# Optimization experiments

Measured on AMD Instinct MI355X. Metric: run time of the kernel, lower is better.

## Reference

```python
import jax, jax.numpy as jnp
import numpy as np

EMBED_DIM = 1024
NUM_HEADS = 16
HEAD_DIM = EMBED_DIM // NUM_HEADS
SCALING = (1.0 / HEAD_DIM) ** 0.5


def setup_inputs() -> dict:
    key = jax.random.key(0)
    ks = jax.random.split(key, 9)
    d = EMBED_DIM
    return {
        "hidden_states": jax.random.normal(ks[0], (4, 2048, d), dtype=jnp.float32),
        "q_w": jax.random.normal(ks[1], (d, d), dtype=jnp.float32) * 0.02,
        "q_b": jax.random.normal(ks[2], (d,), dtype=jnp.float32) * 0.02,
        "k_w": jax.random.normal(ks[3], (d, d), dtype=jnp.float32) * 0.02,
        "k_b": jax.random.normal(ks[4], (d,), dtype=jnp.float32) * 0.02,
        "v_w": jax.random.normal(ks[5], (d, d), dtype=jnp.float32) * 0.02,
        "v_b": jax.random.normal(ks[6], (d,), dtype=jnp.float32) * 0.02,
        "out_w": jax.random.normal(ks[7], (d, d), dtype=jnp.float32) * 0.02,
        "out_b": jax.random.normal(ks[8], (d,), dtype=jnp.float32) * 0.02,
    }


def _shape(x, bsz, seq, nh, hd):
    # [B, T, E] -> [B, H, T, Hd]
    return x.reshape(bsz, seq, nh, hd).transpose(0, 2, 1, 3)


def reference(hidden_states, q_w, q_b, k_w, k_b, v_w, v_b, out_w, out_b):
    bsz, tgt_len, _ = hidden_states.shape
    # torch Linear: y = x @ W.T + b; query scaled by sqrt(1/head_dim)
    q = (hidden_states @ q_w.T + q_b) * SCALING
    k = hidden_states @ k_w.T + k_b
    v = hidden_states @ v_w.T + v_b
    q = _shape(q, bsz, tgt_len, NUM_HEADS, HEAD_DIM)
    k = _shape(k, bsz, tgt_len, NUM_HEADS, HEAD_DIM)
    v = _shape(v, bsz, tgt_len, NUM_HEADS, HEAD_DIM)
    # [B, H, T, S]
    attn_weights = jnp.einsum("bhtd,bhsd->bhts", q, k)
    attn_weights = jax.nn.softmax(attn_weights, axis=-1)
    # [B, H, T, Hd] -> [B, T, E]
    attn_output = jnp.einsum("bhts,bhsd->bhtd", attn_weights, v)
    attn_output = attn_output.transpose(0, 2, 1, 3).reshape(bsz, tgt_len, EMBED_DIM)
    return attn_output @ out_w.T + out_b
```

## Files before the change

### kernel.cpp

```cpp
#include <hip/hip_runtime.h>
#include <hip/hip_bf16.h>
#include <cstdint>
#include <math.h>

typedef uint16_t u16;
typedef __attribute__((ext_vector_type(8))) short short8;
typedef __attribute__((ext_vector_type(2))) float floatx2;
typedef __attribute__((ext_vector_type(4))) float floatx4;
typedef __attribute__((ext_vector_type(16))) float floatx16;

__device__ __forceinline__ float bf2f(u16 u) {
  return __uint_as_float(((uint32_t)u) << 16);
}
__device__ __forceinline__ u16 f2bf(float f) {
  uint32_t u = __float_as_uint(f);
  u += 0x7FFF + ((u >> 16) & 1);
  return (u16)(u >> 16);
}

#if __has_builtin(__builtin_amdgcn_exp2f)
#define EXP2(x) __builtin_amdgcn_exp2f(x)
#else
#define EXP2(x) exp2f(x)
#endif

__device__ __forceinline__ void glds16(const void* g, void* l) {
  __builtin_amdgcn_global_load_lds(
      (const __attribute__((address_space(1))) void*)g,
      (__attribute__((address_space(3))) void*)l, 16, 0, 0);
}

__device__ __forceinline__ bool detect_fp32(const u16* __restrict__ hs) {
  int big = 0;
#pragma unroll
  for (int i = 0; i < 128; ++i) {
    const int e = (hs[i] >> 7) & 0xFF;
    big += (e >= 140);
  }
  return big > 0;
}

__device__ __forceinline__ void conv_blk(
    const void* __restrict__ src, u16* __restrict__ dst, int i, bool f32)
{
  if (f32) {
    const float4 v = ((const float4*)src)[i];
    ushort4 d;
    d.x = f2bf(v.x); d.y = f2bf(v.y); d.z = f2bf(v.z); d.w = f2bf(v.w);
    ((ushort4*)dst)[i] = d;
  } else {
    ((ushort4*)dst)[i] = ((const ushort4*)src)[i];
  }
}

__global__ __launch_bounds__(256) void convert_all(
    const void* __restrict__ hs, const void* __restrict__ qw,
    const void* __restrict__ kw, const void* __restrict__ vw,
    const void* __restrict__ ow, const void* __restrict__ qb,
    const void* __restrict__ kb, const void* __restrict__ vb,
    const void* __restrict__ ob,
    u16* __restrict__ d_hs, u16* __restrict__ d_qw, u16* __restrict__ d_kw,
    u16* __restrict__ d_vw, u16* __restrict__ d_ow, u16* __restrict__ d_qb,
    u16* __restrict__ d_kb, u16* __restrict__ d_vb, u16* __restrict__ d_ob)
{
  const bool f32 = detect_fp32((const u16*)hs);
  const int bid = blockIdx.x;
  const int tid = threadIdx.x;
  if (bid < 2048) {
#pragma unroll
    for (int k = 0; k < 4; ++k)
      conv_blk(hs, d_hs, bid * 1024 + k * 256 + tid, f32);
  } else if (bid < 2048 + 1024) {
    const int w = (bid - 2048) >> 8;
    const int base = ((bid - 2048) & 255) * 1024;
    const void* s = (w == 0) ? qw : (w == 1) ? kw : (w == 2) ? vw : ow;
    u16* d        = (w == 0) ? d_qw : (w == 1) ? d_kw : (w == 2) ? d_vw : d_ow;
#pragma unroll
    for (int k = 0; k < 4; ++k)
      conv_blk(s, d, base + k * 256 + tid, f32);
  } else {
    const int w = bid - 3072;
    const void* s = (w == 0) ? qb : (w == 1) ? kb : (w == 2) ? vb : ob;
    u16* d        = (w == 0) ? d_qb : (w == 1) ? d_kb : (w == 2) ? d_vb : d_ob;
    conv_blk(s, d, tid, f32);
  }
}

template <int MODE>
__device__ __forceinline__ void gemm_body(
    const u16* __restrict__ A, const u16* __restrict__ W,
    const u16* __restrict__ bias, void* __restrict__ vout,
    float scale, u16* As, u16* Bs, int bx, int by, bool f32out)
{
  constexpr int KD = 1024;
  const int tid  = threadIdx.x;
  const int lane = tid & 63;
  const int l15  = lane & 15;
  const int quad = lane >> 4;
  const int wid  = tid >> 6;
  const int bm = by * 256, bn = bx * 128;
  const int wm = (wid >> 1) * 64, wn = (wid & 1) * 64;

  floatx4 acc[4][4];
#pragma unroll
  for (int i = 0; i < 4; ++i)
#pragma unroll
    for (int j = 0; j < 4; ++j)
#pragma unroll
      for (int r = 0; r < 4; ++r) acc[i][j][r] = 0.0f;

  const u16* Ag0 = A + (size_t)(bm + (tid >> 2)) * KD + (tid & 3) * 8;
  const u16* Ag1 = Ag0 + (size_t)128 * KD;
  const u16* Wg0 = W + (size_t)(bn + (tid >> 2)) * KD + (tid & 3) * 8;
  u16* AsD = As + tid * 8;
  u16* BsD = Bs + tid * 8;

  for (int kt = 0; kt < KD / 64; ++kt) {
    const int ko = kt * 64;
    glds16(Ag0 + ko,      AsD);
    glds16(Ag1 + ko,      AsD + 4096);
    glds16(Wg0 + ko,      BsD);
    glds16(Ag0 + ko + 32, AsD + 8192);
    glds16(Ag1 + ko + 32, AsD + 8192 + 4096);
    glds16(Wg0 + ko + 32, BsD + 4096);
    __syncthreads();
#pragma unroll
    for (int h = 0; h < 2; ++h) {
      const u16* Ah = As + h * 8192;
      const u16* Bh = Bs + h * 4096;
      short8 af[4], bf[4];
#pragma unroll
      for (int mb = 0; mb < 4; ++mb)
        af[mb] = *(const short8*)&Ah[(wm + mb * 16 + l15) * 32 + quad * 8];
#pragma unroll
      for (int nb = 0; nb < 4; ++nb)
        bf[nb] = *(const short8*)&Bh[(wn + nb * 16 + l15) * 32 + quad * 8];
#pragma unroll
      for (int mb = 0; mb < 4; ++mb)
#pragma unroll
        for (int nb = 0; nb < 4; ++nb) {
          if (MODE == 2)
            acc[mb][nb] = __builtin_amdgcn_mfma_f32_16x16x32_bf16(
                bf[nb], af[mb], acc[mb][nb], 0, 0, 0);
          else
            acc[mb][nb] = __builtin_amdgcn_mfma_f32_16x16x32_bf16(
                af[mb], bf[nb], acc[mb][nb], 0, 0, 0);
        }
    }
    __syncthreads();
  }

  if (MODE == 2) {
#pragma unroll
    for (int nb = 0; nb < 4; ++nb)
#pragma unroll
      for (int r = 0; r < 4; ++r) {
        const int wrow = bn + wn + nb * 16 + quad * 4 + r;
        const float bv = bf2f(bias[wrow]);
        const int h = wrow >> 6, d = wrow & 63;
        u16* out = (u16*)vout;
#pragma unroll
        for (int mb = 0; mb < 4; ++mb) {
          const int tcol = bm + wm + mb * 16 + l15;
          const int b = tcol >> 11, t = tcol & 2047;
          out[((size_t)(b * 16 + h) * 64 + d) * 2048 + t] =
              f2bf((acc[mb][nb][r] + bv) * scale);
        }
      }
  } else {
    float bias_v[4];
#pragma unroll
    for (int nb = 0; nb < 4; ++nb) bias_v[nb] = bf2f(bias[bn + wn + nb * 16 + l15]);
#pragma unroll
    for (int mb = 0; mb < 4; ++mb)
#pragma unroll
      for (int nb = 0; nb < 4; ++nb)
#pragma unroll
        for (int r = 0; r < 4; ++r) {
          const int row = bm + wm + mb * 16 + quad * 4 + r;
          const int col = bn + wn + nb * 16 + l15;
          const float v = (acc[mb][nb][r] + bias_v[nb]) * scale;
          if (MODE == 0) {
            if (f32out) ((float*)vout)[(size_t)row * 1024 + col] = v;
            else        ((u16*)vout)[(size_t)row * 1024 + col] = f2bf(v);
          } else {
            const int b = row >> 11, t = row & 2047;
            const int h = col >> 6, d = col & 63;
            ((u16*)vout)[(((size_t)(b * 16 + h)) * 2048 + t) * 64 + d] = f2bf(v);
          }
        }
  }
}

__global__ __launch_bounds__(512, 2) void gemm_qkv(
    const u16* __restrict__ A,
    const u16* __restrict__ Wq, const u16* __restrict__ Wk, const u16* __restrict__ Wv,
    const u16* __restrict__ bq, const u16* __restrict__ bk, const u16* __restrict__ bv,
    u16* __restrict__ Oq, u16* __restrict__ Ok, u16* __restrict__ Ov)
{
  __shared__ u16 As[2 * 256 * 32];
  __shared__ u16 Bs[2 * 128 * 32];
  const int lid = blockIdx.x + 8 * blockIdx.y + 256 * blockIdx.z;
  const int w   = (lid & 7) * 96 + (lid >> 3);
  const int bx  = w & 7;
  const int by  = (w >> 3) & 31;
  const int z   = w >> 8;
  if (z < 2) {
    const u16* Wt   = z ? Wk : Wq;
    const u16* bias = z ? bk : bq;
    u16* out        = z ? Ok : Oq;
    const float scale = z ? 1.0f : 0.125f;
    gemm_body<1>(A, Wt, bias, out, scale, As, Bs, bx, by, false);
  } else {
    gemm_body<2>(A, Wv, bv, Ov, 1.0f, As, Bs, bx, by, false);
  }
}

__global__ __launch_bounds__(512, 2) void gemm_out_proj(
    const u16* __restrict__ A, const u16* __restrict__ W,
    const u16* __restrict__ bias, void* __restrict__ out,
    const u16* __restrict__ probe)
{
  __shared__ u16 As[2 * 256 * 32];
  __shared__ u16 Bs[2 * 128 * 32];
  const bool f32 = detect_fp32(probe);
  const int lid = blockIdx.x + 8 * blockIdx.y;
  const int w   = (lid & 7) * 32 + (lid >> 3);
  const int bx  = w & 7;
  const int by  = w >> 3;
  gemm_body<0>(A, W, bias, out, 1.0f, As, Bs, bx, by, f32);
}

__global__ __launch_bounds__(256, 2) void attn_fused(
    const u16* __restrict__ Q, const u16* __restrict__ K,
    const u16* __restrict__ VT, u16* __restrict__ O)
{
  constexpr int T = 2048, D = 64;
  constexpr int KS = 72;
  __shared__ u16 Ks[2][64 * KS];
  __shared__ u16 Vts[2][64 * KS];
  __shared__ float Linv[128];

  const int tid  = threadIdx.x;
  const int lane = tid & 63;
  const int l31  = lane & 31;
  const int half = lane >> 5;
  const int wid  = tid >> 6;
  const int lid = blockIdx.x + 16 * blockIdx.y;
  const int wkid = (lid & 7) * 128 + (lid >> 3);
  const int qt = wkid & 15;
  const int bh = wkid >> 4;
  const int q0w = wid * 32;

  const u16* Qb = Q + (size_t)bh * T * D + (size_t)qt * 128 * D;
  const u16* Kb = K + (size_t)bh * T * D;
  const u16* Vb = VT + (size_t)bh * D * T;

  const int c0r = tid >> 3,        c0o = (tid & 7) * 8;
  const int c1r = (tid + 256) >> 3, c1o = ((tid + 256) & 7) * 8;

  short8 qf[4];
#pragma unroll
  for (int kk = 0; kk < 4; ++kk)
    qf[kk] = *(const short8*)&Qb[(q0w + l31) * D + kk * 16 + half * 8];

  floatx16 o_acc[2];
#pragma unroll
  for (int dt = 0; dt < 2; ++dt)
#pragma unroll
    for (int i = 0; i < 16; ++i) o_acc[dt][i] = 0.0f;
  floatx2 l01 = {0.0f, 0.0f}, l23 = {0.0f, 0.0f};

  const floatx2 L2E2 = {1.4426950408889634f, 1.4426950408889634f};

  short8 krg0, krg1, vrg0, vrg1;
  krg0 = *(const short8*)&Kb[(size_t)c0r * D + c0o];
  krg1 = *(const short8*)&Kb[(size_t)c1r * D + c1o];
  vrg0 = *(const short8*)&Vb[(size_t)c0r * T + c0o];
  vrg1 = *(const short8*)&Vb[(size_t)c1r * T + c1o];

#pragma unroll 1
  for (int kt = 0; kt < T / 64; ++kt) {
    const int cur = kt & 1;
    *(short8*)&Ks[cur][c0r * KS + c0o] = krg0;
    *(short8*)&Ks[cur][c1r * KS + c1o] = krg1;
    *(short8*)&Vts[cur][c0r * KS + c0o] = vrg0;
    *(short8*)&Vts[cur][c1r * KS + c1o] = vrg1;
    __syncthreads();
    if (kt + 1 < T / 64) {
      const u16* Kt = Kb + (size_t)(kt + 1) * 64 * D;
      krg0 = *(const short8*)&Kt[(size_t)c0r * D + c0o];
      krg1 = *(const short8*)&Kt[(size_t)c1r * D + c1o];
      vrg0 = *(const short8*)&Vb[(size_t)c0r * T + (kt + 1) * 64 + c0o];
      vrg1 = *(const short8*)&Vb[(size_t)c1r * T + (kt + 1) * 64 + c1o];
    }

#pragma unroll
    for (int t = 0; t < 2; ++t) {
      floatx16 s;
#pragma unroll
      for (int i = 0; i < 16; ++i) s[i] = 0.0f;
      __builtin_amdgcn_s_setprio(1);
#pragma unroll
      for (int kk = 0; kk < 4; ++kk) {
        const short8 kf =
            *(const short8*)&Ks[cur][(t * 32 + l31) * KS + kk * 16 + half * 8];
        s = __builtin_amdgcn_mfma_f32_32x32x16_bf16(kf, qf[kk], s, 0, 0, 0);
      }
      __builtin_amdgcn_s_setprio(0);
      uint32_t e[4][2];
#pragma unroll
      for (int g = 0; g < 4; ++g) {
        const floatx2 s01 = {s[4 * g + 0], s[4 * g + 1]};
        const floatx2 s23 = {s[4 * g + 2], s[4 * g + 3]};
        floatx2 t01, t23;
        asm("v_pk_mul_f32 %0, %1, %2" : "=v"(t01) : "v"(s01), "v"(L2E2));
        asm("v_pk_mul_f32 %0, %1, %2" : "=v"(t23) : "v"(s23), "v"(L2E2));
        floatx2 p01, p23;
        p01.x = EXP2(fminf(t01.x, 44.f));
        p01.y = EXP2(fminf(t01.y, 44.f));
        p23.x = EXP2(fminf(t23.x, 44.f));
        p23.y = EXP2(fminf(t23.y, 44.f));
        asm("v_pk_add_f32 %0, %0, %1" : "+v"(l01) : "v"(p01));
        asm("v_pk_add_f32 %0, %0, %1" : "+v"(l23) : "v"(p23));
        asm("v_cvt_pk_bf16_f32 %0, %1, %2" : "=v"(e[g][0]) : "v"(p01.x), "v"(p01.y));
        asm("v_cvt_pk_bf16_f32 %0, %1, %2" : "=v"(e[g][1]) : "v"(p23.x), "v"(p23.y));
      }
#pragma unroll
      for (int c = 0; c < 2; ++c) {
        uint32_t a0 = e[2 * c][0], b0 = e[2 * c + 1][0];
        uint32_t a1 = e[2 * c][1], b1 = e[2 * c + 1][1];
        asm("v_permlane32_swap_b32 %0, %1" : "+v"(a0), "+v"(b0));
        asm("v_permlane32_swap_b32 %0, %1" : "+v"(a1), "+v"(b1));
        union { uint32_t u[4]; short8 v; } pu;
        pu.u[0] = a0; pu.u[1] = a1; pu.u[2] = b0; pu.u[3] = b1;
        const short8 pf = pu.v;
        const int kkp = 2 * t + c;
        const short8 vf0 =
            *(const short8*)&Vts[cur][l31 * KS + kkp * 16 + half * 8];
        const short8 vf1 =
            *(const short8*)&Vts[cur][(32 + l31) * KS + kkp * 16 + half * 8];
        __builtin_amdgcn_s_setprio(1);
        o_acc[0] = __builtin_amdgcn_mfma_f32_32x32x16_bf16(pf, vf0, o_acc[0], 0, 0, 0);
        o_acc[1] = __builtin_amdgcn_mfma_f32_32x32x16_bf16(pf, vf1, o_acc[1], 0, 0, 0);
        __builtin_amdgcn_s_setprio(0);
      }
    }
  }

  const float l_acc = (l01.x + l01.y) + (l23.x + l23.y);
  uint32_t lu0 = __float_as_uint(l_acc), lu1 = lu0;
  asm("v_permlane32_swap_b32 %0, %1" : "+v"(lu0), "+v"(lu1));
  const float l_full = l_acc + __uint_as_float(half ? lu0 : lu1);
  __syncthreads();
  Linv[q0w + l31] = 1.0f / l_full;

  const int b = bh >> 4, h = bh & 15;
  u16* Ob = O + ((size_t)b * 2048 + (size_t)qt * 128) * 1024 + h * 64;
  float invs[16];
  __syncthreads();
#pragma unroll
  for (int i = 0; i < 16; ++i)
    invs[i] = Linv[q0w + (i & 3) + 8 * (i >> 2) + 4 * half];
#pragma unroll
  for (int dt = 0; dt < 2; ++dt)
#pragma unroll
    for (int i = 0; i < 16; ++i) {
      const int qrow = q0w + (i & 3) + 8 * (i >> 2) + 4 * half;
      Ob[(size_t)qrow * 1024 + dt * 32 + l31] = f2bf((float)o_acc[dt][i] * invs[i]);
    }
}

extern "C" void kernel_launch(void* const* d_in, const int* in_sizes, int n_in,
                              void* d_out, int out_size, void* d_ws, size_t ws_size,
                              hipStream_t stream) {
  const u16* hs_probe = (const u16*)d_in[0];

  const size_t TE = (size_t)4 * 2048 * 1024;
  const size_t WE = (size_t)1024 * 1024;
  u16* hsB = (u16*)d_ws;
  u16* Qb  = hsB + TE;
  u16* Kb  = Qb + TE;
  u16* Vb  = Kb + TE;
  u16* Ob  = Vb + TE;
  u16* qwB = Ob + TE;
  u16* kwB = qwB + WE;
  u16* vwB = kwB + WE;
  u16* owB = vwB + WE;
  u16* qbB = owB + WE;
  u16* kbB = qbB + 1024;
  u16* vbB = kbB + 1024;
  u16* obB = vbB + 1024;

  dim3 bb(256);
  dim3 gb(512);
  convert_all<<<dim3(3076), bb, 0, stream>>>(
      d_in[0], d_in[1], d_in[3], d_in[5], d_in[7],
      d_in[2], d_in[4], d_in[6], d_in[8],
      hsB, qwB, kwB, vwB, owB, qbB, kbB, vbB, obB);

  gemm_qkv<<<dim3(8, 32, 3), gb, 0, stream>>>(
      hsB, qwB, kwB, vwB, qbB, kbB, vbB, Qb, Kb, Vb);
  attn_fused<<<dim3(16, 64), bb, 0, stream>>>(Qb, Kb, Vb, Ob);
  gemm_out_proj<<<dim3(8, 32), gb, 0, stream>>>(Ob, owB, obB, d_out, hs_probe);
}
```

Before: 287.6 us.

## Split attention key sequence across two wave groups with LDS reduction

Attention blocks grow to 512 threads. Two groups of four waves each process half of the key/value sequence for the same 128 queries, then combine partial outputs and row sums through shared memory before normalising. This doubles the waves working on each query tile, which is meant to raise latency hiding and MFMA utilisation. In exchange it drops the register prefetch double-buffering, loads each tile synchronously behind two barriers per iteration, and adds a reduction epilogue through LDS.

```diff
diff --git a/kernel.cpp b/kernel.cpp
--- a/kernel.cpp
+++ b/kernel.cpp
@@ -231,33 +231,34 @@
   gemm_body<0>(A, W, bias, out, 1.0f, As, Bs, bx, by, f32);
 }
 
-__global__ __launch_bounds__(256, 2) void attn_fused(
+__global__ __launch_bounds__(512, 2) void attn_fused(
     const u16* __restrict__ Q, const u16* __restrict__ K,
     const u16* __restrict__ VT, u16* __restrict__ O)
 {
   constexpr int T = 2048, D = 64;
   constexpr int KS = 72;
-  __shared__ u16 Ks[2][64 * KS];
-  __shared__ u16 Vts[2][64 * KS];
+  __shared__ u16 kvbuf[4][64 * KS];
   __shared__ float Linv[128];
+  __shared__ float Lg1[128];
 
   const int tid  = threadIdx.x;
   const int lane = tid & 63;
   const int l31  = lane & 31;
   const int half = lane >> 5;
   const int wid  = tid >> 6;
+  const int grp  = wid >> 2;
+  const int q0w  = (wid & 3) * 32;
   const int lid = blockIdx.x + 16 * blockIdx.y;
   const int wkid = (lid & 7) * 128 + (lid >> 3);
   const int qt = wkid & 15;
   const int bh = wkid >> 4;
-  const int q0w = wid * 32;
 
   const u16* Qb = Q + (size_t)bh * T * D + (size_t)qt * 128 * D;
   const u16* Kb = K + (size_t)bh * T * D;
   const u16* Vb = VT + (size_t)bh * D * T;
 
-  const int c0r = tid >> 3,        c0o = (tid & 7) * 8;
-  const int c1r = (tid + 256) >> 3, c1o = ((tid + 256) & 7) * 8;
+  const int cr = tid >> 3;
+  const int co = (tid & 7) * 8;
 
   short8 qf[4];
 #pragma unroll
@@ -273,27 +274,22 @@
 
   const floatx2 L2E2 = {1.4426950408889634f, 1.4426950408889634f};
 
-  short8 krg0, krg1, vrg0, vrg1;
-  krg0 = *(const short8*)&Kb[(size_t)c0r * D + c0o];
-  krg1 = *(const short8*)&Kb[(size_t)c1r * D + c1o];
-  vrg0 = *(const short8*)&Vb[(size_t)c0r * T + c0o];
-  vrg1 = *(const short8*)&Vb[(size_t)c1r * T + c1o];
-
 #pragma unroll 1
-  for (int kt = 0; kt < T / 64; ++kt) {
-    const int cur = kt & 1;
-    *(short8*)&Ks[cur][c0r * KS + c0o] = krg0;
-    *(short8*)&Ks[cur][c1r * KS + c1o] = krg1;
-    *(short8*)&Vts[cur][c0r * KS + c0o] = vrg0;
-    *(short8*)&Vts[cur][c1r * KS + c1o] = vrg1;
+  for (int kt = 0; kt < 16; ++kt) {
+    if (kt) __syncthreads();
+    {
+      const u16* Kt0 = Kb + (size_t)(kt * 64) * D;
+      const u16* Kt1 = Kb + (size_t)((kt + 16) * 64) * D;
+      *(short8*)&kvbuf[0][cr * KS + co] = *(const short8*)&Kt0[(size_t)cr * D + co];
+      *(short8*)&kvbuf[1][cr * KS + co] = *(const short8*)&Kt1[(size_t)cr * D + co];
+      *(short8*)&kvbuf[2][cr * KS + co] =
+          *(const short8*)&Vb[(size_t)cr * T + kt * 64 + co];
+      *(short8*)&kvbuf[3][cr * KS + co] =
+          *(const short8*)&Vb[(size_t)cr * T + (kt + 16) * 64 + co];
+    }
     __syncthreads();
-    if (kt + 1 < T / 64) {
-      const u16* Kt = Kb + (size_t)(kt + 1) * 64 * D;
-      krg0 = *(const short8*)&Kt[(size_t)c0r * D + c0o];
-      krg1 = *(const short8*)&Kt[(size_t)c1r * D + c1o];
-      vrg0 = *(const short8*)&Vb[(size_t)c0r * T + (kt + 1) * 64 + c0o];
-      vrg1 = *(const short8*)&Vb[(size_t)c1r * T + (kt + 1) * 64 + c1o];
-    }
+    const u16* Ksg = kvbuf[grp];
+    const u16* Vsg = kvbuf[2 + grp];
 
 #pragma unroll
     for (int t = 0; t < 2; ++t) {
@@ -304,7 +300,7 @@
 #pragma unroll
       for (int kk = 0; kk < 4; ++kk) {
         const short8 kf =
-            *(const short8*)&Ks[cur][(t * 32 + l31) * KS + kk * 16 + half * 8];
+            *(const short8*)&Ksg[(t * 32 + l31) * KS + kk * 16 + half * 8];
         s = __builtin_amdgcn_mfma_f32_32x32x16_bf16(kf, qf[kk], s, 0, 0, 0);
       }
       __builtin_amdgcn_s_setprio(0);
@@ -337,9 +333,9 @@
         const short8 pf = pu.v;
         const int kkp = 2 * t + c;
         const short8 vf0 =
-            *(const short8*)&Vts[cur][l31 * KS + kkp * 16 + half * 8];
+            *(const short8*)&Vsg[l31 * KS + kkp * 16 + half * 8];
         const short8 vf1 =
-            *(const short8*)&Vts[cur][(32 + l31) * KS + kkp * 16 + half * 8];
+            *(const short8*)&Vsg[(32 + l31) * KS + kkp * 16 + half * 8];
         __builtin_amdgcn_s_setprio(1);
         o_acc[0] = __builtin_amdgcn_mfma_f32_32x32x16_bf16(pf, vf0, o_acc[0], 0, 0, 0);
         o_acc[1] = __builtin_amdgcn_mfma_f32_32x32x16_bf16(pf, vf1, o_acc[1], 0, 0, 0);
@@ -352,23 +348,42 @@
   uint32_t lu0 = __float_as_uint(l_acc), lu1 = lu0;
   asm("v_permlane32_swap_b32 %0, %1" : "+v"(lu0), "+v"(lu1));
   const float l_full = l_acc + __uint_as_float(half ? lu0 : lu1);
+
   __syncthreads();
-  Linv[q0w + l31] = 1.0f / l_full;
-
-  const int b = bh >> 4, h = bh & 15;
-  u16* Ob = O + ((size_t)b * 2048 + (size_t)qt * 128) * 1024 + h * 64;
-  float invs[16];
+  float* osc = (float*)&kvbuf[0][0];
+  if (grp == 1) {
+    const int base = ((wid & 3) * 64 + lane) * 33;
+#pragma unroll
+    for (int dt = 0; dt < 2; ++dt)
+#pragma unroll
+      for (int i = 0; i < 16; ++i) osc[base + dt * 16 + i] = o_acc[dt][i];
+    if (half == 0) Lg1[(wid & 3) * 32 + l31] = l_full;
+  }
   __syncthreads();
-#pragma unroll
-  for (int i = 0; i < 16; ++i)
-    invs[i] = Linv[q0w + (i & 3) + 8 * (i >> 2) + 4 * half];
-#pragma unroll
-  for (int dt = 0; dt < 2; ++dt)
-#pragma unroll
-    for (int i = 0; i < 16; ++i) {
-      const int qrow = q0w + (i & 3) + 8 * (i >> 2) + 4 * half;
-      Ob[(size_t)qrow * 1024 + dt * 32 + l31] = f2bf((float)o_acc[dt][i] * invs[i]);
-    }
+  if (grp == 0) {
+    const int base = (wid * 64 + lane) * 33;
+#pragma unroll
+    for (int dt = 0; dt < 2; ++dt)
+#pragma unroll
+      for (int i = 0; i < 16; ++i) o_acc[dt][i] += osc[base + dt * 16 + i];
+    Linv[q0w + l31] = 1.0f / (l_full + Lg1[q0w + l31]);
+  }
+  __syncthreads();
+  if (grp == 0) {
+    const int b = bh >> 4, h = bh & 15;
+    u16* Ob = O + ((size_t)b * 2048 + (size_t)qt * 128) * 1024 + h * 64;
+    float invs[16];
+#pragma unroll
+    for (int i = 0; i < 16; ++i)
+      invs[i] = Linv[q0w + (i & 3) + 8 * (i >> 2) + 4 * half];
+#pragma unroll
+    for (int dt = 0; dt < 2; ++dt)
+#pragma unroll
+      for (int i = 0; i < 16; ++i) {
+        const int qrow = q0w + (i & 3) + 8 * (i >> 2) + 4 * half;
+        Ob[(size_t)qrow * 1024 + dt * 32 + l31] = f2bf((float)o_acc[dt][i] * invs[i]);
+      }
+  }
 }
 
 extern "C" void kernel_launch(void* const* d_in, const int* in_sizes, int n_in,
@@ -401,6 +416,6 @@
 
   gemm_qkv<<<dim3(8, 32, 3), gb, 0, stream>>>(
       hsB, qwB, kwB, vwB, qbB, kbB, vbB, Qb, Kb, Vb);
-  attn_fused<<<dim3(16, 64), bb, 0, stream>>>(Qb, Kb, Vb, Ob);
+  attn_fused<<<dim3(16, 64), gb, 0, stream>>>(Qb, Kb, Vb, Ob);
   gemm_out_proj<<<dim3(8, 32), gb, 0, stream>>>(Ob, owB, obB, d_out, hs_probe);
 }
```

Result: slower. 302.7 us (+5.2%).
